# Performance work log

Hardware: AMD Instinct MI355X
Metric: run time of the kernel (lower is better)

Reference implementation:

```python
import jax, jax.numpy as jnp
import numpy as np

N_GRIDS, N_FEATS = 64, 2
GD = GH = GW = 64
PE_TERMS, N_DIMS = 6, 3
NODES, N_OUT = 64, 1
N_PTS = 524288


def setup_inputs() -> dict:
    key = jax.random.key(0)
    ks = jax.random.split(key, 8)
    x = jax.random.uniform(ks[0], (N_PTS, N_DIMS), jnp.float32, -1.0, 1.0)
    grid_scales = jax.random.uniform(ks[1], (N_GRIDS, 3), jnp.float32, 1.0, 4.0)
    grid_translations = jax.random.uniform(ks[2], (N_GRIDS, 3), jnp.float32, -1.0, 1.0) * (grid_scales - 1.0)
    feature_grids = jax.random.normal(ks[3], (N_GRIDS, N_FEATS, GD, GH, GW), jnp.float32)
    d_in = PE_TERMS * N_DIMS * 2 + N_FEATS * N_GRIDS  # 36 + 128 = 164
    W0 = jax.random.normal(ks[4], (d_in, NODES), jnp.float32) * np.sqrt(2.0 / (d_in + NODES))
    b0 = jnp.zeros((NODES,), jnp.float32)
    W1 = jax.random.normal(ks[5], (NODES, NODES), jnp.float32) * np.sqrt(2.0 / (2 * NODES))
    b1 = jnp.zeros((NODES,), jnp.float32)
    W2 = jax.random.normal(ks[6], (NODES, N_OUT), jnp.float32) * np.sqrt(2.0 / (NODES + N_OUT))
    b2 = jnp.zeros((N_OUT,), jnp.float32)
    return dict(x=x, grid_scales=grid_scales, grid_translations=grid_translations,
                feature_grids=feature_grids, W0=W0, b0=b0, W1=W1, b1=b1, W2=W2, b2=b2)


def grid_sample_3d(vol, coords):
    """Trilinear grid_sample, align_corners=True, padding_mode='zeros'.
    vol: [C,D,H,W]; coords: [N,3] in (x,y,z) order (x -> W axis), range [-1,1].
    Returns [C,N]."""
    C, D, H, W = vol.shape
    flat = vol.reshape(C, D * H * W)
    ix = (coords[:, 0] + 1.0) * 0.5 * (W - 1)
    iy = (coords[:, 1] + 1.0) * 0.5 * (H - 1)
    iz = (coords[:, 2] + 1.0) * 0.5 * (D - 1)
    x0 = jnp.floor(ix); y0 = jnp.floor(iy); z0 = jnp.floor(iz)
    wx = ix - x0; wy = iy - y0; wz = iz - z0
    x0i = x0.astype(jnp.int32); y0i = y0.astype(jnp.int32); z0i = z0.astype(jnp.int32)
    out = jnp.zeros((C, coords.shape[0]), vol.dtype)
    for dz, wz_ in ((0, 1.0 - wz), (1, wz)):
        for dy, wy_ in ((0, 1.0 - wy), (1, wy)):
            for dx, wx_ in ((0, 1.0 - wx), (1, wx)):
                xi = x0i + dx; yi = y0i + dy; zi = z0i + dz
                valid = (xi >= 0) & (xi < W) & (yi >= 0) & (yi < H) & (zi >= 0) & (zi < D)
                idx = (jnp.clip(zi, 0, D - 1) * H + jnp.clip(yi, 0, H - 1)) * W + jnp.clip(xi, 0, W - 1)
                v = jnp.take(flat, idx, axis=1) * valid.astype(vol.dtype)[None, :]
                out = out + v * (wz_ * wy_ * wx_)[None, :]
    return out


def positional_encoding(x):
    # NeRF-style PE: sin/cos of pi*2^i * x, i in [0, PE_TERMS), out dim = 2*L*3
    freqs = jnp.pi * (2.0 ** jnp.arange(PE_TERMS, dtype=jnp.float32))  # [L]
    ang = x[:, None, :] * freqs[None, :, None]                          # [N,L,3]
    n = x.shape[0]
    return jnp.concatenate([jnp.sin(ang).reshape(n, -1), jnp.cos(ang).reshape(n, -1)], axis=1)


def snake_alt(x):
    return 0.5 * x + jnp.sin(x) ** 2


def reference(x, grid_scales, grid_translations, feature_grids, W0, b0, W1, b1, W2, b2):
    # per-grid affine transform (equivalent to bmm with the scale+translation 4x4)
    tp = x[None, :, :] * grid_scales[:, None, :] + grid_translations[:, None, :]  # [G,N,3]
    feats = jax.vmap(grid_sample_3d)(feature_grids, tp)  # [G,C,N]
    G, C, N = feats.shape
    feats = feats.reshape(G * C, N).T                    # [N, G*C]
    pe = positional_encoding(x)                          # [N, 2*L*3]
    y = jnp.concatenate([pe, feats], axis=1)
    y = snake_alt(y @ W0 + b0)
    y = snake_alt(y @ W1 + b1)
    y = y @ W2 + b2
    return y
```

## Files before the change

kernel.cpp:

```cpp
#include <hip/hip_runtime.h>
#include <hip/hip_bf16.h>

#define NPTS    524288
#define NG      64
#define GSZ     64
#define VOX     (GSZ*GSZ*GSZ)
#define NODES   64
#define TILE    64
#define NBLK    (NPTS / TILE)
#define K0      192
#define SF      200
#define WLCAP   2048
#define NCELL   4096
#define PREP_VB 16384
#define PREP_CB 2048

typedef __attribute__((ext_vector_type(8))) short bf16x8;
typedef __attribute__((ext_vector_type(4))) float f32x4;

__device__ inline unsigned short f2bf(float f) {
    __hip_bfloat16 b = __float2bfloat16(f);
    union { __hip_bfloat16 h; unsigned short u; } cv; cv.h = b;
    return cv.u;
}
__device__ inline unsigned int pk2(float c0, float c1) {
    return (unsigned int)f2bf(c0) | ((unsigned int)f2bf(c1) << 16);
}
__device__ inline float bflo(unsigned int v) { return __uint_as_float(v << 16); }
__device__ inline float bfhi(unsigned int v) { return __uint_as_float(v & 0xffff0000u); }

__device__ inline int spread4(int v) {
    return (v & 1) | ((v & 2) << 2) | ((v & 4) << 4) | ((v & 8) << 6);
}
__device__ inline int cell_of(float px, float py, float pz) {
    int cx = min(max((int)((px + 1.0f) * 8.0f), 0), 15);
    int cy = min(max((int)((py + 1.0f) * 8.0f), 0), 15);
    int cz = min(max((int)((pz + 1.0f) * 8.0f), 0), 15);
    return spread4(cx) | (spread4(cy) << 1) | (spread4(cz) << 2);
}


__global__ void prep_fused(const float* __restrict__ fg, uint4* __restrict__ vox4,
                           const float* __restrict__ x, unsigned short* __restrict__ cid,
                           int* __restrict__ hist,
                           const float* __restrict__ W0, const float* __restrict__ W1,
                           unsigned short* __restrict__ w0t, unsigned short* __restrict__ w1t) {
    int b = blockIdx.x;
    int tid = threadIdx.x;
    if (b < PREP_VB) {
        int idx = b * 256 + tid;
        int g = idx >> 16;
        int hb = idx & 65535;
        int brick = hb >> 1;
        int h = hb & 1;
        int bx = brick & 31, by = (brick >> 5) & 31, bz = brick >> 10;
        int xx = bx << 1, yy = by << 1, zz = (bz << 1) + h;
        const float* c0 = fg + (size_t)g * (2 * VOX) + ((zz << 6) + yy) * 64 + xx;
        const float* c1 = c0 + VOX;
        float2 a0 = *(const float2*)c0;
        float2 a1 = *(const float2*)(c0 + 64);
        float2 d0 = *(const float2*)c1;
        float2 d1 = *(const float2*)(c1 + 64);
        vox4[idx] = make_uint4(pk2(a0.x, d0.x), pk2(a0.y, d0.y),
                               pk2(a1.x, d1.x), pk2(a1.y, d1.y));
    } else if (b < PREP_VB + PREP_CB) {
        int p = (b - PREP_VB) * 256 + tid;
        int c = cell_of(x[p * 3 + 0], x[p * 3 + 1], x[p * 3 + 2]);
        cid[p] = (unsigned short)c;
        atomicAdd(&hist[c], 1);
    } else {
        int t = (b - PREP_VB - PREP_CB) * 256 + tid;
        for (int i = t; i < NODES * K0; i += 4096) {
            int n = i / K0, k = i - n * K0;
            w0t[i] = (k < 164) ? f2bf(W0[k * NODES + n]) : (unsigned short)0;
        }
        for (int i = t; i < NODES * NODES; i += 4096) {
            int n = i >> 6, k = i & 63;
            w1t[i] = f2bf(W1[k * NODES + n]);
        }
    }
}

__global__ void sort_scan(const int* __restrict__ hist, int* __restrict__ offs) {
    __shared__ int partial[256];
    int t = threadIdx.x;
    int loc[16];
    int s = 0;
    #pragma unroll
    for (int i = 0; i < 16; ++i) { loc[i] = s; s += hist[t * 16 + i]; }
    partial[t] = s;
    __syncthreads();
    for (int d = 1; d < 256; d <<= 1) {
        int v = (t >= d) ? partial[t - d] : 0;
        __syncthreads();
        partial[t] += v;
        __syncthreads();
    }
    int base = partial[t] - s;
    #pragma unroll
    for (int i = 0; i < 16; ++i) offs[t * 16 + i] = base + loc[i];
}

__global__ void sort_scatter(const float* __restrict__ x, const unsigned short* __restrict__ cell_id,
                             int* __restrict__ offs, float4* __restrict__ spts) {
    int p = blockIdx.x * blockDim.x + threadIdx.x;
    int c = cell_id[p];
    int pos = atomicAdd(&offs[c], 1);
    spts[pos] = make_float4(x[p * 3 + 0], x[p * 3 + 1], x[p * 3 + 2], __int_as_float(p));
}

__device__ inline void gather_pair(int pt, int g,
                                   const unsigned int* __restrict__ vox,
                                   const float* xs, const float* gss, const float* gts,
                                   unsigned short* Fsh) {
    float px = xs[pt * 3 + 0], py = xs[pt * 3 + 1], pz = xs[pt * 3 + 2];
    float ix = (px * gss[g * 3 + 0] + gts[g * 3 + 0] + 1.0f) * 31.5f;
    float iy = (py * gss[g * 3 + 1] + gts[g * 3 + 1] + 1.0f) * 31.5f;
    float iz = (pz * gss[g * 3 + 2] + gts[g * 3 + 2] + 1.0f) * 31.5f;
    float fx = floorf(ix), fy = floorf(iy), fz = floorf(iz);
    int x0 = (int)fx, y0 = (int)fy, z0 = (int)fz;
    float wx = ix - fx, wy = iy - fy, wz = iz - fz;
    float wxa0 = (x0 >= 0) ? (1.0f - wx) : 0.0f;
    float wxa1 = (x0 < 63) ? wx : 0.0f;
    float wya0 = (y0 >= 0) ? (1.0f - wy) : 0.0f;
    float wya1 = (y0 < 63) ? wy : 0.0f;
    float wza0 = (z0 >= 0) ? (1.0f - wz) : 0.0f;
    float wza1 = (z0 < 63) ? wz : 0.0f;
    int xc0 = max(x0, 0), xc1 = min(x0 + 1, 63);
    int yc0 = max(y0, 0), yc1 = min(y0 + 1, 63);
    int zc0 = max(z0, 0), zc1 = min(z0 + 1, 63);
    int xp0 = ((xc0 >> 1) << 3) | (xc0 & 1);
    int xp1 = ((xc1 >> 1) << 3) | (xc1 & 1);
    int yp0 = ((yc0 >> 1) << 8) | ((yc0 & 1) << 1);
    int yp1 = ((yc1 >> 1) << 8) | ((yc1 & 1) << 1);
    int zp0 = ((zc0 >> 1) << 13) | ((zc0 & 1) << 2);
    int zp1 = ((zc1 >> 1) << 13) | ((zc1 & 1) << 2);
    const unsigned int* vg = vox + ((size_t)g << 18);
    float f0 = 0.f, f1 = 0.f;
    #pragma unroll
    for (int dz = 0; dz < 2; ++dz) {
        int zp = dz ? zp1 : zp0; float wzv = dz ? wza1 : wza0;
        #pragma unroll
        for (int dy = 0; dy < 2; ++dy) {
            int rowb = zp + (dy ? yp1 : yp0);
            float wzy = wzv * (dy ? wya1 : wya0);
            unsigned int v0 = vg[rowb + xp0], v1 = vg[rowb + xp1];
            f0 += wzy * (wxa0 * bflo(v0) + wxa1 * bflo(v1));
            f1 += wzy * (wxa0 * bfhi(v0) + wxa1 * bfhi(v1));
        }
    }
    *(unsigned int*)&Fsh[pt * SF + 36 + 2 * g] = pk2(f0, f1);
}

__global__ void __launch_bounds__(256, 5)
amrsrn_main(const float4* __restrict__ spts,
            const float* __restrict__ gscale,
            const float* __restrict__ gtrans,
            const unsigned int* __restrict__ vox,
            const unsigned short* __restrict__ w0t,
            const unsigned short* __restrict__ w1t,
            const float* __restrict__ b0,
            const float* __restrict__ b1,
            const float* __restrict__ W2,
            const float* __restrict__ b2,
            float* __restrict__ out) {
    __shared__ unsigned short Fsh[TILE * SF];
    __shared__ unsigned short wl[WLCAP];
    __shared__ float xs[TILE * 3];
    __shared__ int   sidx[TILE];
    __shared__ float gss[NG * 3];
    __shared__ float gts[NG * 3];
    __shared__ int wl_cnt;

    const int tid = threadIdx.x;
    const int lane = tid & 63;
    const int cb = ((blockIdx.x & 7) << 10) | (blockIdx.x >> 3);
    const int base = cb * TILE;

    for (int i = tid; i < TILE * SF / 8; i += 256) ((uint4*)Fsh)[i] = make_uint4(0,0,0,0);
    if (tid < TILE) {
        float4 sp = spts[base + tid];
        xs[tid * 3 + 0] = sp.x; xs[tid * 3 + 1] = sp.y; xs[tid * 3 + 2] = sp.z;
        sidx[tid] = __float_as_int(sp.w);
    }
    if (tid < NG * 3) { gss[tid] = gscale[tid]; gts[tid] = gtrans[tid]; }
    if (tid == 0) wl_cnt = 0;
    __syncthreads();

    {
        int pt = tid & 63;
        int grp = tid >> 6;
        #pragma unroll
        for (int t = 0; t < 9; ++t) {
            int tau = grp * 9 + t;
            int tt = (tau < 18) ? tau : tau - 18;
            int l = tt / 3, d = tt - l * 3;
            float ang = xs[pt * 3 + d] * (3.14159265358979323846f * (float)(1 << l));
            float val = (tau < 18) ? __sinf(ang) : __cosf(ang);
            Fsh[pt * SF + tau] = f2bf(val);
        }
    }

    {
        int pt = tid & 63;
        int gbase = (tid >> 6) * 16;
        float px = xs[pt * 3 + 0], py = xs[pt * 3 + 1], pz = xs[pt * 3 + 2];
        for (int gi = 0; gi < 16; ++gi) {
            int g = gbase + gi;
            float ix = (px * gss[g * 3 + 0] + gts[g * 3 + 0] + 1.0f) * 31.5f;
            float iy = (py * gss[g * 3 + 1] + gts[g * 3 + 1] + 1.0f) * 31.5f;
            float iz = (pz * gss[g * 3 + 2] + gts[g * 3 + 2] + 1.0f) * 31.5f;
            bool valid = (ix >= -1.0f) & (ix < 64.0f)
                       & (iy >= -1.0f) & (iy < 64.0f)
                       & (iz >= -1.0f) & (iz < 64.0f);
            unsigned long long m = __ballot(valid);
            if (m) {
                int b = 0;
                if (lane == 0) b = atomicAdd(&wl_cnt, __popcll(m));
                b = __shfl(b, 0);
                if (valid) {
                    int slot = b + __popcll(m & ((1ull << lane) - 1ull));
                    if (slot < WLCAP) wl[slot] = (unsigned short)((pt << 6) | g);
                    else gather_pair(pt, g, vox, xs, gss, gts, Fsh);
                }
            }
        }
    }
    __syncthreads();

    {
        int n = min(wl_cnt, WLCAP);
        for (int i = tid; i < n; i += 256) {
            int e = wl[i];
            gather_pair(e >> 6, e & 63, vox, xs, gss, gts, Fsh);
        }
    }
    __syncthreads();

    const int wv = tid >> 6;
    const int ptb = wv * 16;
    const int row = lane & 15;
    const int quad = lane >> 4;
    const int koff = quad * 8;

    f32x4 acc0[4] = {{0,0,0,0},{0,0,0,0},{0,0,0,0},{0,0,0,0}};
    #pragma unroll
    for (int ks = 0; ks < 6; ++ks) {
        bf16x8 a = *(const bf16x8*)&Fsh[(ptb + row) * SF + ks * 32 + koff];
        #pragma unroll
        for (int nt = 0; nt < 4; ++nt) {
            bf16x8 b = *(const bf16x8*)&w0t[(nt * 16 + row) * K0 + ks * 32 + koff];
            acc0[nt] = __builtin_amdgcn_mfma_f32_16x16x32_bf16(a, b, acc0[nt], 0, 0, 0);
        }
    }
    #pragma unroll
    for (int nt = 0; nt < 4; ++nt) {
        int node = nt * 16 + row;
        float bb = b0[node];
        #pragma unroll
        for (int r = 0; r < 4; ++r) {
            float h = acc0[nt][r] + bb;
            float s = __sinf(h);
            h = 0.5f * h + s * s;
            Fsh[(ptb + quad * 4 + r) * SF + node] = f2bf(h);
        }
    }

    f32x4 acc1[4] = {{0,0,0,0},{0,0,0,0},{0,0,0,0},{0,0,0,0}};
    #pragma unroll
    for (int ks = 0; ks < 2; ++ks) {
        bf16x8 a = *(const bf16x8*)&Fsh[(ptb + row) * SF + ks * 32 + koff];
        #pragma unroll
        for (int nt = 0; nt < 4; ++nt) {
            bf16x8 b = *(const bf16x8*)&w1t[(nt * 16 + row) * NODES + ks * 32 + koff];
            acc1[nt] = __builtin_amdgcn_mfma_f32_16x16x32_bf16(a, b, acc1[nt], 0, 0, 0);
        }
    }
    float part[4] = {0.f, 0.f, 0.f, 0.f};
    #pragma unroll
    for (int nt = 0; nt < 4; ++nt) {
        int node = nt * 16 + row;
        float b1v = b1[node];
        float w2v = W2[node];
        #pragma unroll
        for (int r = 0; r < 4; ++r) {
            float h = acc1[nt][r] + b1v;
            float s = __sinf(h);
            h = 0.5f * h + s * s;
            part[r] += h * w2v;
        }
    }
    #pragma unroll
    for (int m = 1; m < 16; m <<= 1) {
        #pragma unroll
        for (int r = 0; r < 4; ++r) part[r] += __shfl_xor(part[r], m);
    }
    if (row == 0) {
        float b2v = b2[0];
        #pragma unroll
        for (int r = 0; r < 4; ++r) {
            int pt = ptb + quad * 4 + r;
            out[sidx[pt]] = part[r] + b2v;
        }
    }
}

__global__ void amrsrn_fallback(const float* __restrict__ x,
                                const float* __restrict__ gscale,
                                const float* __restrict__ gtrans,
                                const float* __restrict__ fg,
                                const float* __restrict__ W0,
                                const float* __restrict__ b0,
                                const float* __restrict__ W1,
                                const float* __restrict__ b1,
                                const float* __restrict__ W2,
                                const float* __restrict__ b2,
                                float* __restrict__ out) {
    int p = blockIdx.x * blockDim.x + threadIdx.x;
    float px = x[p*3+0], py = x[p*3+1], pz = x[p*3+2];
    float h0[NODES];
    #pragma unroll
    for (int j = 0; j < NODES; ++j) h0[j] = b0[j];
    #pragma unroll
    for (int l = 0; l < 6; ++l) {
        float freq = 3.14159265358979323846f * (float)(1 << l);
        #pragma unroll
        for (int d = 0; d < 3; ++d) {
            float v = (d == 0 ? px : (d == 1 ? py : pz)) * freq;
            float s = __sinf(v), c = __cosf(v);
            const float* wrs = W0 + (l*3 + d) * NODES;
            const float* wrc = W0 + (18 + l*3 + d) * NODES;
            #pragma unroll
            for (int j = 0; j < NODES; ++j) h0[j] += s * wrs[j] + c * wrc[j];
        }
    }
    for (int g = 0; g < NG; ++g) {
        float ix = (px * gscale[g*3+0] + gtrans[g*3+0] + 1.0f) * 31.5f;
        float iy = (py * gscale[g*3+1] + gtrans[g*3+1] + 1.0f) * 31.5f;
        float iz = (pz * gscale[g*3+2] + gtrans[g*3+2] + 1.0f) * 31.5f;
        float fxf = floorf(ix), fyf = floorf(iy), fzf = floorf(iz);
        int x0 = (int)fxf, y0 = (int)fyf, z0 = (int)fzf;
        float wx = ix - fxf, wy = iy - fyf, wz = iz - fzf;
        bool any = (x0 >= -1 && x0 < GSZ) && (y0 >= -1 && y0 < GSZ) && (z0 >= -1 && z0 < GSZ);
        if (any) {
            float f0 = 0.f, f1 = 0.f;
            #pragma unroll
            for (int dz = 0; dz < 2; ++dz) {
                int zi = z0 + dz; bool vz = ((unsigned)zi < (unsigned)GSZ);
                int zc = min(max(zi, 0), GSZ - 1);
                float wzf = dz ? wz : 1.f - wz;
                #pragma unroll
                for (int dy = 0; dy < 2; ++dy) {
                    int yi = y0 + dy; bool vy = ((unsigned)yi < (unsigned)GSZ);
                    int yc = min(max(yi, 0), GSZ - 1);
                    float wyf = dy ? wy : 1.f - wy;
                    int rowoff = (zc * GSZ + yc) * GSZ;
                    #pragma unroll
                    for (int dx = 0; dx < 2; ++dx) {
                        int xi = x0 + dx; bool vx = ((unsigned)xi < (unsigned)GSZ);
                        int xc = min(max(xi, 0), GSZ - 1);
                        float w = wzf * wyf * (dx ? wx : 1.f - wx);
                        w = (vz && vy && vx) ? w : 0.f;
                        const float* gp = fg + ((size_t)g << 19);
                        f0 += w * gp[rowoff + xc];
                        f1 += w * gp[VOX + rowoff + xc];
                    }
                }
            }
            const float* wr = W0 + (36 + 2*g) * NODES;
            #pragma unroll
            for (int j = 0; j < NODES; ++j) h0[j] += f0 * wr[j] + f1 * wr[NODES + j];
        }
    }
    #pragma unroll
    for (int j = 0; j < NODES; ++j) { float s = __sinf(h0[j]); h0[j] = 0.5f * h0[j] + s * s; }
    float out_acc = b2[0];
    #pragma unroll
    for (int half = 0; half < 2; ++half) {
        float h1[32];
        #pragma unroll
        for (int j = 0; j < 32; ++j) h1[j] = b1[half*32 + j];
        #pragma unroll
        for (int i = 0; i < NODES; ++i) {
            float a = h0[i];
            const float* w1r = W1 + i * NODES + half*32;
            #pragma unroll
            for (int j = 0; j < 32; ++j) h1[j] += a * w1r[j];
        }
        #pragma unroll
        for (int j = 0; j < 32; ++j) { float s = __sinf(h1[j]); out_acc += (0.5f * h1[j] + s * s) * W2[half*32 + j]; }
    }
    out[p] = out_acc;
}

extern "C" void kernel_launch(void* const* d_in, const int* in_sizes, int n_in,
                              void* d_out, int out_size, void* d_ws, size_t ws_size,
                              hipStream_t stream) {
    const float* x      = (const float*)d_in[0];
    const float* gscale = (const float*)d_in[1];
    const float* gtrans = (const float*)d_in[2];
    const float* fg     = (const float*)d_in[3];
    const float* W0     = (const float*)d_in[4];
    const float* b0     = (const float*)d_in[5];
    const float* W1     = (const float*)d_in[6];
    const float* b1     = (const float*)d_in[7];
    const float* W2     = (const float*)d_in[8];
    const float* b2     = (const float*)d_in[9];
    float* out = (float*)d_out;

    char* wsp = (char*)d_ws;
    unsigned short* w0t = (unsigned short*)wsp;
    unsigned short* w1t = w0t + NODES * K0;
    int* hist           = (int*)(wsp + (64 << 10));
    int* offs           = (int*)(wsp + (80 << 10));
    unsigned short* cid = (unsigned short*)(wsp + (96 << 10));
    float4* spts        = (float4*)(wsp + (96 << 10) + (1 << 20));
    unsigned int* vox   = (unsigned int*)(wsp + (96 << 10) + (1 << 20) + (8 << 20));
    const size_t ws_needed = (96 << 10) + (1 << 20) + (8 << 20) + (size_t)NG * VOX * 4;

    if (ws_size >= ws_needed) {
        hipMemsetAsync(hist, 0, NCELL * sizeof(int), stream);
        prep_fused<<<PREP_VB + PREP_CB + 16, 256, 0, stream>>>(
            fg, (uint4*)vox, x, cid, hist, W0, W1, w0t, w1t);
        sort_scan<<<1, 256, 0, stream>>>(hist, offs);
        sort_scatter<<<NPTS / 256, 256, 0, stream>>>(x, cid, offs, spts);
        amrsrn_main<<<NBLK, 256, 0, stream>>>(spts, gscale, gtrans, vox,
                                              w0t, w1t, b0, b1, W2, b2, out);
    } else {
        amrsrn_fallback<<<NPTS / 256, 256, 0, stream>>>(
            x, gscale, gtrans, fg, W0, b0, W1, b1, W2, b2, out);
    }
}
```

Before: 449.4 us.

## Replace LDS worklist gather with per-tile bounding-box grid classification

Each wave computes the bounding box of its 64 spatially sorted points with shuffle reductions, then classifies every grid as fully inside, partially overlapping, or entirely outside that box. Grids that are fully inside or partial are handed round-robin to the four waves, and each lane gathers its own point, so validity checks are skipped for fully-inside grids and grids outside the box are skipped entirely. This removes the shared-memory worklist with its atomics, one barrier and the LDS copy of point coordinates. In exchange, each wave's lanes always do a full 64-point gather per grid, and partial grids still need a per-lane validity check, which causes divergence.

```diff
diff --git a/kernel.cpp b/kernel.cpp
--- a/kernel.cpp
+++ b/kernel.cpp
@@ -10,7 +10,6 @@
 #define NBLK    (NPTS / TILE)
 #define K0      192
 #define SF      200
-#define WLCAP   2048
 #define NCELL   4096
 #define PREP_VB 16384
 #define PREP_CB 2048
@@ -109,14 +108,9 @@
     spts[pos] = make_float4(x[p * 3 + 0], x[p * 3 + 1], x[p * 3 + 2], __int_as_float(p));
 }
 
-__device__ inline void gather_pair(int pt, int g,
+__device__ inline void gather_pair(int pt, int g, float ix, float iy, float iz,
                                    const unsigned int* __restrict__ vox,
-                                   const float* xs, const float* gss, const float* gts,
                                    unsigned short* Fsh) {
-    float px = xs[pt * 3 + 0], py = xs[pt * 3 + 1], pz = xs[pt * 3 + 2];
-    float ix = (px * gss[g * 3 + 0] + gts[g * 3 + 0] + 1.0f) * 31.5f;
-    float iy = (py * gss[g * 3 + 1] + gts[g * 3 + 1] + 1.0f) * 31.5f;
-    float iz = (pz * gss[g * 3 + 2] + gts[g * 3 + 2] + 1.0f) * 31.5f;
     float fx = floorf(ix), fy = floorf(iy), fz = floorf(iz);
     int x0 = (int)fx, y0 = (int)fy, z0 = (int)fz;
     float wx = ix - fx, wy = iy - fy, wz = iz - fz;
@@ -165,79 +159,91 @@
             const float* __restrict__ b2,
             float* __restrict__ out) {
     __shared__ unsigned short Fsh[TILE * SF];
-    __shared__ unsigned short wl[WLCAP];
-    __shared__ float xs[TILE * 3];
     __shared__ int   sidx[TILE];
     __shared__ float gss[NG * 3];
     __shared__ float gts[NG * 3];
-    __shared__ int wl_cnt;
 
     const int tid = threadIdx.x;
     const int lane = tid & 63;
+    const int wv = tid >> 6;
     const int cb = ((blockIdx.x & 7) << 10) | (blockIdx.x >> 3);
     const int base = cb * TILE;
 
     for (int i = tid; i < TILE * SF / 8; i += 256) ((uint4*)Fsh)[i] = make_uint4(0,0,0,0);
-    if (tid < TILE) {
-        float4 sp = spts[base + tid];
-        xs[tid * 3 + 0] = sp.x; xs[tid * 3 + 1] = sp.y; xs[tid * 3 + 2] = sp.z;
-        sidx[tid] = __float_as_int(sp.w);
-    }
+    float4 sp = spts[base + lane];
+    const float px = sp.x, py = sp.y, pz = sp.z;
+    if (tid < TILE) sidx[tid] = __float_as_int(sp.w);
     if (tid < NG * 3) { gss[tid] = gscale[tid]; gts[tid] = gtrans[tid]; }
-    if (tid == 0) wl_cnt = 0;
     __syncthreads();
 
+    float lox = px, hix = px, loy = py, hiy = py, loz = pz, hiz = pz;
+    #pragma unroll
+    for (int m = 1; m < 64; m <<= 1) {
+        lox = fminf(lox, __shfl_xor(lox, m)); hix = fmaxf(hix, __shfl_xor(hix, m));
+        loy = fminf(loy, __shfl_xor(loy, m)); hiy = fmaxf(hiy, __shfl_xor(hiy, m));
+        loz = fminf(loz, __shfl_xor(loz, m)); hiz = fmaxf(hiz, __shfl_xor(hiz, m));
+    }
+    unsigned long long mfull, mpart;
     {
-        int pt = tid & 63;
-        int grp = tid >> 6;
+        int g = lane;
+        float s0 = gss[g*3+0], s1 = gss[g*3+1], s2 = gss[g*3+2];
+        float t0 = gts[g*3+0], t1 = gts[g*3+1], t2 = gts[g*3+2];
+        float xl = (lox*s0 + t0 + 1.0f)*31.5f, xh = (hix*s0 + t0 + 1.0f)*31.5f;
+        float yl = (loy*s1 + t1 + 1.0f)*31.5f, yh = (hiy*s1 + t1 + 1.0f)*31.5f;
+        float zl = (loz*s2 + t2 + 1.0f)*31.5f, zh = (hiz*s2 + t2 + 1.0f)*31.5f;
+        bool fullg = (xl >= -0.999f) & (xh <= 63.999f)
+                   & (yl >= -0.999f) & (yh <= 63.999f)
+                   & (zl >= -0.999f) & (zh <= 63.999f);
+        bool outg  = (xh < -1.001f) | (xl >= 64.001f)
+                   | (yh < -1.001f) | (yl >= 64.001f)
+                   | (zh < -1.001f) | (zl >= 64.001f);
+        mfull = __ballot(fullg);
+        mpart = __ballot(!fullg && !outg);
+    }
+
+    {
         #pragma unroll
         for (int t = 0; t < 9; ++t) {
-            int tau = grp * 9 + t;
+            int tau = wv * 9 + t;
             int tt = (tau < 18) ? tau : tau - 18;
             int l = tt / 3, d = tt - l * 3;
-            float ang = xs[pt * 3 + d] * (3.14159265358979323846f * (float)(1 << l));
+            float c = (d == 0) ? px : ((d == 1) ? py : pz);
+            float ang = c * (3.14159265358979323846f * (float)(1 << l));
             float val = (tau < 18) ? __sinf(ang) : __cosf(ang);
-            Fsh[pt * SF + tau] = f2bf(val);
+            Fsh[lane * SF + tau] = f2bf(val);
         }
     }
 
     {
-        int pt = tid & 63;
-        int gbase = (tid >> 6) * 16;
-        float px = xs[pt * 3 + 0], py = xs[pt * 3 + 1], pz = xs[pt * 3 + 2];
-        for (int gi = 0; gi < 16; ++gi) {
-            int g = gbase + gi;
-            float ix = (px * gss[g * 3 + 0] + gts[g * 3 + 0] + 1.0f) * 31.5f;
-            float iy = (py * gss[g * 3 + 1] + gts[g * 3 + 1] + 1.0f) * 31.5f;
-            float iz = (pz * gss[g * 3 + 2] + gts[g * 3 + 2] + 1.0f) * 31.5f;
-            bool valid = (ix >= -1.0f) & (ix < 64.0f)
-                       & (iy >= -1.0f) & (iy < 64.0f)
-                       & (iz >= -1.0f) & (iz < 64.0f);
-            unsigned long long m = __ballot(valid);
-            if (m) {
-                int b = 0;
-                if (lane == 0) b = atomicAdd(&wl_cnt, __popcll(m));
-                b = __shfl(b, 0);
-                if (valid) {
-                    int slot = b + __popcll(m & ((1ull << lane) - 1ull));
-                    if (slot < WLCAP) wl[slot] = (unsigned short)((pt << 6) | g);
-                    else gather_pair(pt, g, vox, xs, gss, gts, Fsh);
-                }
+        int idx = 0;
+        unsigned long long m = mfull;
+        while (m) {
+            int g = __builtin_ctzll(m);
+            m &= m - 1;
+            if ((idx++ & 3) == wv) {
+                float ix = (px * gss[g*3+0] + gts[g*3+0] + 1.0f) * 31.5f;
+                float iy = (py * gss[g*3+1] + gts[g*3+1] + 1.0f) * 31.5f;
+                float iz = (pz * gss[g*3+2] + gts[g*3+2] + 1.0f) * 31.5f;
+                gather_pair(lane, g, ix, iy, iz, vox, Fsh);
             }
         }
+        m = mpart;
+        while (m) {
+            int g = __builtin_ctzll(m);
+            m &= m - 1;
+            if ((idx++ & 3) == wv) {
+                float ix = (px * gss[g*3+0] + gts[g*3+0] + 1.0f) * 31.5f;
+                float iy = (py * gss[g*3+1] + gts[g*3+1] + 1.0f) * 31.5f;
+                float iz = (pz * gss[g*3+2] + gts[g*3+2] + 1.0f) * 31.5f;
+                bool valid = (ix >= -1.0f) & (ix < 64.0f)
+                           & (iy >= -1.0f) & (iy < 64.0f)
+                           & (iz >= -1.0f) & (iz < 64.0f);
+                if (valid) gather_pair(lane, g, ix, iy, iz, vox, Fsh);
+            }
+        }
     }
     __syncthreads();
 
-    {
-        int n = min(wl_cnt, WLCAP);
-        for (int i = tid; i < n; i += 256) {
-            int e = wl[i];
-            gather_pair(e >> 6, e & 63, vox, xs, gss, gts, Fsh);
-        }
-    }
-    __syncthreads();
-
-    const int wv = tid >> 6;
     const int ptb = wv * 16;
     const int row = lane & 15;
     const int quad = lane >> 4;
```

Result: no change. 448.4 us (-0.2%).
